# Performance work log

Measured on AMD Instinct MI355X. Metric: run time of the kernel, lower is better.

## Reference

```python
import jax, jax.numpy as jnp
import numpy as np
import itertools

RANKS_HIGH = 15
SUITS_HIGH = 5
B, M = 16, 24
# Omaha unspool: choose 2 of 4 hole cards x choose 3 of 5 board cards -> 60 five-card combos
COMBOS = np.array([h + b for h in itertools.combinations(range(4), 2)
                   for b in itertools.combinations(range(4, 9), 3)], dtype=np.int32)  # [60, 5]


def setup_inputs() -> dict:
    key = jax.random.key(0)
    ks = list(jax.random.split(key, 20))
    f = lambda i, shape: jax.random.normal(ks[i], shape, jnp.float32) * 0.05
    ranks = jax.random.randint(ks[0], (B, M, 9), 2, RANKS_HIGH)  # card ranks 2..14
    suits = jax.random.randint(ks[1], (B, M, 9), 1, SUITS_HIGH)  # suits 1..4
    x = jnp.stack([ranks, suits], axis=-1).reshape(B, M, 18)     # alternating rank/suit
    ones16 = jnp.ones((16,), jnp.float32)
    zeros16 = jnp.zeros((16,), jnp.float32)
    return {
        "x": x,
        "suit_w": f(2, (16, 5, 1)), "suit_b": f(3, (16,)),
        "rank_w": f(4, (16, 5, 5)), "rank_b": f(5, (16,)),
        "bn_s_gamma": ones16, "bn_s_beta": zeros16, "bn_s_mean": zeros16, "bn_s_var": ones16,
        "bn_r_gamma": ones16, "bn_r_beta": zeros16, "bn_r_mean": zeros16, "bn_r_var": ones16,
        "w1": f(6, (32, 16)), "b1": f(7, (32,)),
        "w2": f(8, (32, 32)), "b2": f(9, (32,)),
        "wc": f(10, (7463, 512)), "bc": f(11, (7463,)),
        "wo1": f(12, (512, 15360)), "bo1": f(13, (512,)),
        "wo2": f(14, (256, 512)), "bo2": f(15, (256,)),
        "wo3": f(16, (127, 256)), "bo3": f(17, (127,)),
    }


def _bn(t, gamma, beta, mean, var, eps=1e-5):
    # eval-mode BatchNorm1d; channel axis is -2 (shape [..., 16, L])
    inv = gamma / jnp.sqrt(var + eps)
    return t * inv[:, None] + (beta - mean * inv)[:, None]


def _forward(x, suit_w, suit_b, bn_s_gamma, bn_s_beta, bn_s_mean, bn_s_var,
             rank_w, rank_b, bn_r_gamma, bn_r_beta, bn_r_mean, bn_r_var,
             w1, b1, w2, b2, wc, bc, wo1, bo1, wo2, bo2, wo3, bo3):
    b, m, _ = x.shape
    ranks = x[..., 0::2][..., COMBOS]  # [B,M,60,5]
    suits = x[..., 1::2][..., COMBOS]  # [B,M,60,5]
    hot_r = jax.nn.one_hot(ranks, RANKS_HIGH, dtype=jnp.float32)  # [B,M,60,5,15]
    hot_s = jax.nn.one_hot(suits, SUITS_HIGH, dtype=jnp.float32)  # [B,M,60,5,5]
    # suit conv: Conv1d(5,16,k=1) over the one-hot length; channels = 5 cards
    s = jnp.einsum('bmkcl,oc->bmkol', hot_s, suit_w[:, :, 0]) + suit_b[:, None]
    s = jax.nn.relu(_bn(s, bn_s_gamma, bn_s_beta, bn_s_mean, bn_s_var))  # [B,M,60,16,5]
    # rank conv: Conv1d(5,16,k=5) valid: length 15 -> 11
    n = b * m * 60
    r = jax.lax.conv_general_dilated(hot_r.reshape(n, 5, RANKS_HIGH), rank_w,
                                     window_strides=(1,), padding='VALID',
                                     dimension_numbers=('NCH', 'OIH', 'NCH'))
    r = r.reshape(b, m, 60, 16, 11) + rank_b[:, None]
    r = jax.nn.relu(_bn(r, bn_r_gamma, bn_r_beta, bn_r_mean, bn_r_var))  # [B,M,60,16,11]
    raw = jnp.concatenate([r, s], axis=-1)  # [B,M,60,16,16]
    # hand-class head: two hidden linears on last dim, then 512 -> 7463
    h = jax.nn.relu(raw @ w1.T + b1)        # [B,M,60,16,32]
    h = jax.nn.relu(h @ w2.T + b2)          # [B,M,60,16,32]
    logits = h.reshape(b, m, 60, 512) @ wc.T + bc  # [B,M,60,7463]
    best = jnp.min(jnp.argmax(jax.lax.stop_gradient(logits), axis=-1),
                   axis=-1, keepdims=True)  # [B,M,1] (lower class index = better hand)
    # raw-feature head: [B,M,60*16*16=15360] -> 512 -> 256 -> 127
    o = raw.reshape(b, m, 60 * 16 * 16)
    o = jax.nn.relu(o @ wo1.T + bo1)
    o = jax.nn.relu(o @ wo2.T + bo2)
    o = jax.nn.relu(o @ wo3.T + bo3)
    return jnp.concatenate([o, best.astype(o.dtype)], axis=-1)  # [B,M,128]


def reference(x, suit_w, suit_b, bn_s_gamma, bn_s_beta, bn_s_mean, bn_s_var,
              rank_w, rank_b, bn_r_gamma, bn_r_beta, bn_r_mean, bn_r_var,
              w1, b1, w2, b2, wc, bc, wo1, bo1, wo2, bo2, wo3, bo3):
    return _forward(x, suit_w, suit_b, bn_s_gamma, bn_s_beta, bn_s_mean, bn_s_var,
                    rank_w, rank_b, bn_r_gamma, bn_r_beta, bn_r_mean, bn_r_var,
                    w1, b1, w2, b2, wc, bc, wo1, bo1, wo2, bo2, wo3, bo3)
```

## Files before the change

kernel.cpp:

```cpp
#include <hip/hip_runtime.h>

#define NSAMP 384
#define NCOMBO 60
#define NROW 23040
#define KDIM 512
#define NCLS 7463
#define NCLSP 7680
#define NTILE_N 60
#define NTILE_M 180
#define O1_NZ 30
#define O1_KZ 512

typedef short s16x8 __attribute__((ext_vector_type(8)));
typedef short s16x4 __attribute__((ext_vector_type(4)));
typedef float f32x4 __attribute__((ext_vector_type(4)));

__device__ unsigned short g_wc_hi[NCLSP * KDIM];
__device__ unsigned short g_wc_lo[NCLSP * KDIM];
__device__ unsigned short g_h_hi[NROW * KDIM];
__device__ unsigned short g_h_lo[NROW * KDIM];
__device__ unsigned short g_rawbf[NROW * 256];
__device__ unsigned short g_wo1bf[512 * 15360];
__device__ float          g_pmax[NTILE_N * NROW];
__device__ int            g_pidx[NTILE_N * NROW];
__device__ float          g_part[O1_NZ * NSAMP * 512];

__device__ __forceinline__ float bf2f(unsigned short u){
  union { unsigned int i; float f; } v; v.i = ((unsigned int)u) << 16; return v.f;
}
__device__ __forceinline__ unsigned short f2bf(float f){
  union { float f; unsigned int i; } v; v.f = f;
  unsigned int u = v.i;
  unsigned int r = (u + 0x7FFFu + ((u >> 16) & 1u)) >> 16;
  return (unsigned short)r;
}
__device__ __forceinline__ void gload16(const void* g, void* l){
  __builtin_amdgcn_global_load_lds((const __attribute__((address_space(1))) void*)g,
                                   (__attribute__((address_space(3))) void*)l, 16, 0, 0);
}

__global__ __launch_bounds__(256) void k_split(const float* __restrict__ wc)
{
  int idx = (blockIdx.x * 256 + threadIdx.x) * 4;
  float4 w = {0.f, 0.f, 0.f, 0.f};
  if (idx < NCLS * KDIM) w = *(const float4*)(wc + idx);
  s16x4 hi, lo;
  float wv[4] = {w.x, w.y, w.z, w.w};
  #pragma unroll
  for (int i = 0; i < 4; ++i){
    unsigned short h = f2bf(wv[i]);
    hi[i] = (short)h;
    lo[i] = (short)f2bf(wv[i] - bf2f(h));
  }
  *(s16x4*)(g_wc_hi + idx) = hi;
  *(s16x4*)(g_wc_lo + idx) = lo;
}

__global__ __launch_bounds__(256) void k_splitw(const float* __restrict__ wo1)
{
  int idx = (blockIdx.x * 256 + threadIdx.x) * 4;
  float4 w = *(const float4*)(wo1 + idx);
  s16x4 b;
  b[0] = (short)f2bf(w.x); b[1] = (short)f2bf(w.y);
  b[2] = (short)f2bf(w.z); b[3] = (short)f2bf(w.w);
  *(s16x4*)(g_wo1bf + idx) = b;
}

__global__ __launch_bounds__(256) void k_features(
    const int* __restrict__ x,
    const float* __restrict__ suit_w, const float* __restrict__ suit_b,
    const float* __restrict__ rank_w, const float* __restrict__ rank_b,
    const float* __restrict__ bns_g, const float* __restrict__ bns_b,
    const float* __restrict__ bns_m, const float* __restrict__ bns_v,
    const float* __restrict__ bnr_g, const float* __restrict__ bnr_b,
    const float* __restrict__ bnr_m, const float* __restrict__ bnr_v,
    const float* __restrict__ w1, const float* __restrict__ b1,
    const float* __restrict__ w2, const float* __restrict__ b2)
{
  __shared__ float raw_s[4][256];
  __shared__ float h1_s[4][512];
  const int tid  = threadIdx.x;
  const int lane = tid & 63;
  const int wv   = tid >> 6;
  const int combo = blockIdx.x * 4 + wv;
  const int s = combo / 60;
  const int k = combo % 60;
  const int hp = k / 10, bt = k % 10;
  const int HP0[6]  = {0,0,0,1,1,2}, HP1[6] = {1,2,3,2,3,3};
  const int BT0[10] = {4,4,4,4,4,4,5,5,5,6};
  const int BT1[10] = {5,5,5,6,6,7,6,6,7,7};
  const int BT2[10] = {6,7,8,7,8,8,7,8,8,8};
  int cards[5] = {HP0[hp], HP1[hp], BT0[bt], BT1[bt], BT2[bt]};
  const int* xp = x + s * 18;
  int rk[5], st[5];
  #pragma unroll
  for (int c = 0; c < 5; ++c){ rk[c] = xp[2*cards[c]]; st[c] = xp[2*cards[c] + 1]; }

  {
    s16x4 rv;
    #pragma unroll
    for (int i = 0; i < 4; ++i){
      int e = lane * 4 + i;
      int o = e >> 4, l = e & 15;
      float v;
      if (l < 11){
        float a = 0.f;
        #pragma unroll
        for (int c = 0; c < 5; ++c){
          int d = rk[c] - l;
          if (d >= 0 && d < 5) a += rank_w[o*25 + c*5 + d];
        }
        a += rank_b[o];
        float inv = bnr_g[o] / sqrtf(bnr_v[o] + 1e-5f);
        v = a * inv + (bnr_b[o] - bnr_m[o] * inv);
      } else {
        int j = l - 11;
        float a = suit_b[o];
        #pragma unroll
        for (int c = 0; c < 5; ++c) if (st[c] == j) a += suit_w[o*5 + c];
        float inv = bns_g[o] / sqrtf(bns_v[o] + 1e-5f);
        v = a * inv + (bns_b[o] - bns_m[o] * inv);
      }
      v = fmaxf(v, 0.f);
      raw_s[wv][e] = v;
      rv[i] = (short)f2bf(v);
    }
    *(s16x4*)(g_rawbf + (size_t)s * 15360 + k * 256 + lane * 4) = rv;
  }
  __syncthreads();
  #pragma unroll
  for (int i = 0; i < 8; ++i){
    int e = lane + 64 * i;
    int o = e >> 5, j = e & 31;
    float a = b1[j];
    #pragma unroll
    for (int l = 0; l < 16; ++l) a += raw_s[wv][o*16 + l] * w1[j*16 + l];
    h1_s[wv][e] = fmaxf(a, 0.f);
  }
  __syncthreads();
  {
    s16x8 hv, lv;
    #pragma unroll
    for (int i = 0; i < 8; ++i){
      int e = lane * 8 + i;
      int o = e >> 5, j = e & 31;
      float a = b2[j];
      #pragma unroll
      for (int l = 0; l < 32; ++l) a += h1_s[wv][o*32 + l] * w2[j*32 + l];
      a = fmaxf(a, 0.f);
      unsigned short h = f2bf(a);
      hv[i] = (short)h;
      lv[i] = (short)f2bf(a - bf2f(h));
    }
    *(s16x8*)(g_h_hi + (size_t)combo * 512 + lane * 8) = hv;
    *(s16x8*)(g_h_lo + (size_t)combo * 512 + lane * 8) = lv;
  }
}

__global__ __launch_bounds__(256, 2) void k_logits(const float* __restrict__ bc)
{
  __shared__ unsigned char lds[65536];
  const int tid  = threadIdx.x;
  const int lane = tid & 63;
  const int wv   = tid >> 6;
  const int wr   = wv >> 1, wq = wv & 1;
  const int flat  = blockIdx.x;
  const int xcd   = flat & 7;
  const int seq   = flat >> 3;
  const int group = xcd >> 1;
  const int par   = xcd & 1;
  const int mt    = (seq / 15) * 2 + par;
  const int nt    = group * 15 + (seq % 15);
  const int m0 = mt * 128;
  const int n0 = nt * 128;

  f32x4 acc[4][4];
  #pragma unroll
  for (int i = 0; i < 4; ++i)
    #pragma unroll
    for (int j = 0; j < 4; ++j)
      acc[i][j] = (f32x4){0.f, 0.f, 0.f, 0.f};

  const int rA = lane >> 2;
  const int c0 = lane & 3;

  auto stage = [&](int b, int kc){
    unsigned base = b * 32768;
    #pragma unroll
    for (int it = 0; it < 2; ++it){
      int seg = wv * 2 + it;
      int r   = seg * 16 + rA;
      int cs  = c0 ^ ((rA >> 1) & 3);
      size_t gA = (size_t)(m0 + r) * KDIM + kc + cs * 8;
      size_t gB = (size_t)(n0 + r) * KDIM + kc + cs * 8;
      unsigned lb = base + seg * 1024;
      gload16(g_h_hi  + gA, lds + lb);
      gload16(g_h_lo  + gA, lds + lb + 8192);
      gload16(g_wc_hi + gB, lds + lb + 16384);
      gload16(g_wc_lo + gB, lds + lb + 24576);
    }
  };

  int buf = 0;
  stage(0, 0);
  __syncthreads();
  for (int t = 0; t < 16; ++t){
    if (t < 15) stage(buf ^ 1, (t + 1) * 32);
    unsigned base = buf * 32768;
    const int q = lane >> 4;
    s16x8 a_h[4], a_l[4];
    #pragma unroll
    for (int i = 0; i < 4; ++i){
      int row = wr * 64 + i * 16 + (lane & 15);
      unsigned off = base + row * 64 + ((q ^ ((row >> 1) & 3)) * 16);
      a_h[i] = *(const s16x8*)(lds + off);
      a_l[i] = *(const s16x8*)(lds + off + 8192);
    }
    #pragma unroll
    for (int j = 0; j < 4; ++j){
      int col = wq * 64 + j * 16 + (lane & 15);
      unsigned off = base + col * 64 + ((q ^ ((col >> 1) & 3)) * 16);
      s16x8 b_h = *(const s16x8*)(lds + off + 16384);
      s16x8 b_l = *(const s16x8*)(lds + off + 24576);
      #pragma unroll
      for (int i = 0; i < 4; ++i){
        acc[i][j] = __builtin_amdgcn_mfma_f32_16x16x32_bf16(a_h[i], b_h, acc[i][j], 0, 0, 0);
        acc[i][j] = __builtin_amdgcn_mfma_f32_16x16x32_bf16(a_h[i], b_l, acc[i][j], 0, 0, 0);
        acc[i][j] = __builtin_amdgcn_mfma_f32_16x16x32_bf16(a_l[i], b_h, acc[i][j], 0, 0, 0);
      }
    }
    __syncthreads();
    buf ^= 1;
  }
  float* cmax = (float*)lds;
  int*   cidx = (int*)(lds + 1024);
  const int g = lane >> 4;
  #pragma unroll
  for (int i = 0; i < 4; ++i){
    #pragma unroll
    for (int r = 0; r < 4; ++r){
      float bv = -__builtin_inff(); int bi = 0x7FFFFFFF;
      #pragma unroll
      for (int j = 0; j < 4; ++j){
        int col = n0 + wq * 64 + j * 16 + (lane & 15);
        if (col < NCLS){
          float v = acc[i][j][r] + bc[col];
          if (v > bv){ bv = v; bi = col; }
        }
      }
      for (int s = 1; s < 16; s <<= 1){
        float ov = __shfl_xor(bv, s);
        int   oi = __shfl_xor(bi, s);
        if (ov > bv || (ov == bv && oi < bi)){ bv = ov; bi = oi; }
      }
      if ((lane & 15) == 0){
        int rloc = wr * 64 + i * 16 + g * 4 + r;
        cmax[rloc * 2 + wq] = bv;
        cidx[rloc * 2 + wq] = bi;
      }
    }
  }
  __syncthreads();
  if (tid < 128){
    float bv = cmax[tid * 2];     int bi = cidx[tid * 2];
    float v1 = cmax[tid * 2 + 1]; int i1 = cidx[tid * 2 + 1];
    if (v1 > bv || (v1 == bv && i1 < bi)){ bv = v1; bi = i1; }
    size_t row = (size_t)(m0 + tid);
    g_pmax[(size_t)nt * NROW + row] = bv;
    g_pidx[(size_t)nt * NROW + row] = bi;
  }
}

__global__ __launch_bounds__(64) void k_best(float* __restrict__ out)
{
  __shared__ int bis[60];
  const int s = blockIdx.x; const int t = threadIdx.x;
  if (t < 60){
    size_t row = (size_t)s * 60 + t;
    float bv = -__builtin_inff(); int bi = 0x7FFFFFFF;
    for (int q = 0; q < NTILE_N; ++q){
      float v = g_pmax[(size_t)q * NROW + row];
      int   i = g_pidx[(size_t)q * NROW + row];
      if (v > bv || (v == bv && i < bi)){ bv = v; bi = i; }
    }
    bis[t] = bi;
  }
  __syncthreads();
  if (t == 0){
    int m = bis[0];
    for (int i = 1; i < 60; ++i) m = min(m, bis[i]);
    out[s * 128 + 127] = (float)m;
  }
}

__global__ __launch_bounds__(256) void k_o1(void)
{
  __shared__ unsigned char As[16384];
  __shared__ unsigned char Bs[16384];
  const int tid  = threadIdx.x;
  const int lane = tid & 63;
  const int wv   = tid >> 6;
  const int wr   = wv >> 1, wq = wv & 1;
  const int n0  = blockIdx.x * 128;
  const int m0  = blockIdx.y * 128;
  const int kc0 = blockIdx.z * O1_KZ;

  f32x4 acc[4][4];
  #pragma unroll
  for (int i = 0; i < 4; ++i)
    #pragma unroll
    for (int j = 0; j < 4; ++j)
      acc[i][j] = (f32x4){0.f, 0.f, 0.f, 0.f};

  const int rA = lane >> 3;
  const int c0 = lane & 7;
  for (int kk = 0; kk < O1_KZ; kk += 64){
    int kc = kc0 + kk;
    __syncthreads();
    #pragma unroll
    for (int it = 0; it < 4; ++it){
      int seg = wv * 4 + it;
      int r   = seg * 8 + rA;
      int cs  = c0 ^ (r & 7);
      gload16(g_rawbf + (size_t)(m0 + r) * 15360 + kc + cs * 8, As + seg * 1024);
      gload16(g_wo1bf + (size_t)(n0 + r) * 15360 + kc + cs * 8, Bs + seg * 1024);
    }
    __syncthreads();
    #pragma unroll
    for (int ks = 0; ks < 2; ++ks){
      int q = ks * 4 + (lane >> 4);
      s16x8 a[4];
      #pragma unroll
      for (int i = 0; i < 4; ++i){
        int row = wr * 64 + i * 16 + (lane & 15);
        a[i] = *(const s16x8*)(As + row * 128 + ((q ^ (row & 7)) * 16));
      }
      #pragma unroll
      for (int j = 0; j < 4; ++j){
        int col = wq * 64 + j * 16 + (lane & 15);
        s16x8 b = *(const s16x8*)(Bs + col * 128 + ((q ^ (col & 7)) * 16));
        #pragma unroll
        for (int i = 0; i < 4; ++i)
          acc[i][j] = __builtin_amdgcn_mfma_f32_16x16x32_bf16(a[i], b, acc[i][j], 0, 0, 0);
      }
    }
  }
  const int g = lane >> 4;
  #pragma unroll
  for (int i = 0; i < 4; ++i)
    #pragma unroll
    for (int j = 0; j < 4; ++j)
      #pragma unroll
      for (int r = 0; r < 4; ++r){
        int gm = m0 + wr * 64 + i * 16 + g * 4 + r;
        int gn = n0 + wq * 64 + j * 16 + (lane & 15);
        g_part[((size_t)blockIdx.z * NSAMP + gm) * 512 + gn] = acc[i][j][r];
      }
}

__global__ __launch_bounds__(256) void k_otail(
    const float* __restrict__ bo1, const float* __restrict__ wo2,
    const float* __restrict__ bo2, const float* __restrict__ wo3,
    const float* __restrict__ bo3, float* __restrict__ out)
{
  __shared__ float o1f[512];
  __shared__ float o2f[256];
  const int s = blockIdx.x;
  const int tid = threadIdx.x;
  for (int j = tid; j < 512; j += 256){
    float a = bo1[j];
    for (int ks = 0; ks < O1_NZ; ++ks) a += g_part[((size_t)ks * NSAMP + s) * 512 + j];
    o1f[j] = fmaxf(a, 0.f);
  }
  __syncthreads();
  {
    float a = bo2[tid];
    const float* wr = wo2 + (size_t)tid * 512;
    for (int i = 0; i < 512; i += 4){
      float4 w4 = *(const float4*)(wr + i);
      a += o1f[i]*w4.x + o1f[i+1]*w4.y + o1f[i+2]*w4.z + o1f[i+3]*w4.w;
    }
    o2f[tid] = fmaxf(a, 0.f);
  }
  __syncthreads();
  if (tid < 127){
    float a = bo3[tid];
    const float* wr = wo3 + (size_t)tid * 256;
    for (int i = 0; i < 256; i += 4){
      float4 w4 = *(const float4*)(wr + i);
      a += o2f[i]*w4.x + o2f[i+1]*w4.y + o2f[i+2]*w4.z + o2f[i+3]*w4.w;
    }
    out[s * 128 + tid] = fmaxf(a, 0.f);
  }
}

extern "C" void kernel_launch(void* const* d_in, const int* in_sizes, int n_in,
                              void* d_out, int out_size, void* d_ws, size_t ws_size,
                              hipStream_t stream)
{
  (void)d_ws; (void)ws_size; (void)in_sizes; (void)n_in; (void)out_size;
  const int*   x      = (const int*)  d_in[0];
  const float* suit_w = (const float*)d_in[1];
  const float* suit_b = (const float*)d_in[2];
  const float* rank_w = (const float*)d_in[3];
  const float* rank_b = (const float*)d_in[4];
  const float* bns_g  = (const float*)d_in[5];
  const float* bns_b  = (const float*)d_in[6];
  const float* bns_m  = (const float*)d_in[7];
  const float* bns_v  = (const float*)d_in[8];
  const float* bnr_g  = (const float*)d_in[9];
  const float* bnr_b  = (const float*)d_in[10];
  const float* bnr_m  = (const float*)d_in[11];
  const float* bnr_v  = (const float*)d_in[12];
  const float* w1     = (const float*)d_in[13];
  const float* b1     = (const float*)d_in[14];
  const float* w2     = (const float*)d_in[15];
  const float* b2     = (const float*)d_in[16];
  const float* wc     = (const float*)d_in[17];
  const float* bc     = (const float*)d_in[18];
  const float* wo1    = (const float*)d_in[19];
  const float* bo1    = (const float*)d_in[20];
  const float* wo2    = (const float*)d_in[21];
  const float* bo2    = (const float*)d_in[22];
  const float* wo3    = (const float*)d_in[23];
  const float* bo3    = (const float*)d_in[24];
  float* out = (float*)d_out;

  hipLaunchKernelGGL(k_split,  dim3(3840), dim3(256), 0, stream, wc);
  hipLaunchKernelGGL(k_splitw, dim3(7680), dim3(256), 0, stream, wo1);
  hipLaunchKernelGGL(k_features, dim3(5760), dim3(256), 0, stream, x,
                     suit_w, suit_b, rank_w, rank_b,
                     bns_g, bns_b, bns_m, bns_v, bnr_g, bnr_b, bnr_m, bnr_v,
                     w1, b1, w2, b2);
  hipLaunchKernelGGL(k_logits, dim3(NTILE_N * NTILE_M), dim3(256), 0, stream, bc);
  hipLaunchKernelGGL(k_best, dim3(NSAMP), dim3(64), 0, stream, out);
  hipLaunchKernelGGL(k_o1, dim3(4, 3, O1_NZ), dim3(256), 0, stream);
  hipLaunchKernelGGL(k_otail, dim3(NSAMP), dim3(256), 0, stream,
                     bo1, wo2, bo2, wo3, bo3, out);
}
```

Baseline: 1.158 ms.

## Enlarge logits GEMM tiles to 256x256 with 8 waves and split-bf16 as K-extension

The logits GEMM moves from 128x128 tiles with 4 waves to 256x256 tiles with 8 waves. The three bf16 hi/lo partial products are recast as a K dimension three times as long (48 steps), so each step does one MFMA per fragment pair instead of staging hi and lo buffers together. Pipelining now uses explicit vmcnt waits, raw s_barrier and setprio around the MFMA block, and the argmax reduction is widened to four column waves. The goal is more operand reuse per LDS byte and less global traffic. In exchange there is higher register pressure from 32 accumulators per lane, and 2700 blocks of 512 threads may fill the CUs unevenly.

Result: no change. 1.156 ms (-0.2%).

```diff
diff --git a/kernel.cpp b/kernel.cpp
--- a/kernel.cpp
+++ b/kernel.cpp
@@ -6,8 +6,8 @@
 #define KDIM 512
 #define NCLS 7463
 #define NCLSP 7680
-#define NTILE_N 60
-#define NTILE_M 180
+#define NTILE_N 30
+#define NTILE_M 90
 #define O1_NZ 30
 #define O1_KZ 512
 
@@ -157,92 +157,102 @@
   }
 }
 
-__global__ __launch_bounds__(256, 2) void k_logits(const float* __restrict__ bc)
+__global__ __launch_bounds__(512, 2) void k_logits(const float* __restrict__ bc)
 {
   __shared__ unsigned char lds[65536];
   const int tid  = threadIdx.x;
   const int lane = tid & 63;
   const int wv   = tid >> 6;
-  const int wr   = wv >> 1, wq = wv & 1;
-  const int flat  = blockIdx.x;
-  const int xcd   = flat & 7;
-  const int seq   = flat >> 3;
-  const int group = xcd >> 1;
-  const int par   = xcd & 1;
-  const int mt    = (seq / 15) * 2 + par;
-  const int nt    = group * 15 + (seq % 15);
-  const int m0 = mt * 128;
-  const int n0 = nt * 128;
-
-  f32x4 acc[4][4];
-  #pragma unroll
-  for (int i = 0; i < 4; ++i)
+  const int wm   = wv >> 2, wn = wv & 3;
+  const int blk  = blockIdx.x;
+  const int nt   = blk / NTILE_M;
+  const int mt   = blk % NTILE_M;
+  const int m0 = mt * 256;
+  const int n0 = nt * 256;
+
+  f32x4 acc[8][4];
+  #pragma unroll
+  for (int i = 0; i < 8; ++i)
     #pragma unroll
     for (int j = 0; j < 4; ++j)
       acc[i][j] = (f32x4){0.f, 0.f, 0.f, 0.f};
 
-  const int rA = lane >> 2;
-  const int c0 = lane & 3;
-
-  auto stage = [&](int b, int kc){
-    unsigned base = b * 32768;
+  const int sR0 = tid >> 2;
+  const int sCS = (tid & 3) ^ ((tid >> 3) & 3);
+  auto stage = [&](int buf, int t){
+    const int seg = t >> 4;
+    const int kc  = (t & 15) * 32;
+    const unsigned short* As = (seg < 2) ? g_h_hi : g_h_lo;
+    const unsigned short* Bs = (seg == 1) ? g_wc_lo : g_wc_hi;
+    const unsigned base = buf * 32768;
     #pragma unroll
     for (int it = 0; it < 2; ++it){
-      int seg = wv * 2 + it;
-      int r   = seg * 16 + rA;
-      int cs  = c0 ^ ((rA >> 1) & 3);
-      size_t gA = (size_t)(m0 + r) * KDIM + kc + cs * 8;
-      size_t gB = (size_t)(n0 + r) * KDIM + kc + cs * 8;
-      unsigned lb = base + seg * 1024;
-      gload16(g_h_hi  + gA, lds + lb);
-      gload16(g_h_lo  + gA, lds + lb + 8192);
-      gload16(g_wc_hi + gB, lds + lb + 16384);
-      gload16(g_wc_lo + gB, lds + lb + 24576);
+      int R = it * 128 + sR0;
+      gload16(As + (size_t)(m0 + R) * KDIM + kc + sCS * 8,
+              lds + base + it * 8192 + wv * 1024);
+    }
+    #pragma unroll
+    for (int it = 0; it < 2; ++it){
+      int R = it * 128 + sR0;
+      gload16(Bs + (size_t)(n0 + R) * KDIM + kc + sCS * 8,
+              lds + base + 16384 + it * 8192 + wv * 1024);
     }
   };
 
-  int buf = 0;
   stage(0, 0);
-  __syncthreads();
-  for (int t = 0; t < 16; ++t){
-    if (t < 15) stage(buf ^ 1, (t + 1) * 32);
-    unsigned base = buf * 32768;
-    const int q = lane >> 4;
-    s16x8 a_h[4], a_l[4];
-    #pragma unroll
-    for (int i = 0; i < 4; ++i){
-      int row = wr * 64 + i * 16 + (lane & 15);
-      unsigned off = base + row * 64 + ((q ^ ((row >> 1) & 3)) * 16);
-      a_h[i] = *(const s16x8*)(lds + off);
-      a_l[i] = *(const s16x8*)(lds + off + 8192);
+  stage(1, 1);
+  asm volatile("s_waitcnt vmcnt(4)" ::: "memory");
+  __builtin_amdgcn_sched_barrier(0);
+  __builtin_amdgcn_s_barrier();
+  asm volatile("" ::: "memory");
+
+  const int q = lane >> 4;
+  #pragma unroll 1
+  for (int t = 0; t < 48; ++t){
+    const unsigned cb = (unsigned)(t & 1) * 32768;
+    s16x8 af[8], bf[4];
+    #pragma unroll
+    for (int i = 0; i < 8; ++i){
+      int row = wm * 128 + i * 16 + (lane & 15);
+      af[i] = *(const s16x8*)(lds + cb + row * 64 + ((q ^ ((row >> 1) & 3)) << 4));
     }
     #pragma unroll
     for (int j = 0; j < 4; ++j){
-      int col = wq * 64 + j * 16 + (lane & 15);
-      unsigned off = base + col * 64 + ((q ^ ((col >> 1) & 3)) * 16);
-      s16x8 b_h = *(const s16x8*)(lds + off + 16384);
-      s16x8 b_l = *(const s16x8*)(lds + off + 24576);
-      #pragma unroll
-      for (int i = 0; i < 4; ++i){
-        acc[i][j] = __builtin_amdgcn_mfma_f32_16x16x32_bf16(a_h[i], b_h, acc[i][j], 0, 0, 0);
-        acc[i][j] = __builtin_amdgcn_mfma_f32_16x16x32_bf16(a_h[i], b_l, acc[i][j], 0, 0, 0);
-        acc[i][j] = __builtin_amdgcn_mfma_f32_16x16x32_bf16(a_l[i], b_h, acc[i][j], 0, 0, 0);
-      }
-    }
-    __syncthreads();
-    buf ^= 1;
-  }
+      int row = wn * 64 + j * 16 + (lane & 15);
+      bf[j] = *(const s16x8*)(lds + cb + 16384 + row * 64 + ((q ^ ((row >> 1) & 3)) << 4));
+    }
+    __builtin_amdgcn_s_setprio(1);
+    #pragma unroll
+    for (int i = 0; i < 8; ++i)
+      #pragma unroll
+      for (int j = 0; j < 4; ++j)
+        acc[i][j] = __builtin_amdgcn_mfma_f32_16x16x32_bf16(af[i], bf[j], acc[i][j], 0, 0, 0);
+    __builtin_amdgcn_s_setprio(0);
+    __builtin_amdgcn_sched_barrier(0);
+    __builtin_amdgcn_s_barrier();
+    asm volatile("" ::: "memory");
+    if (t + 2 < 48){
+      stage(t & 1, t + 2);
+      asm volatile("s_waitcnt vmcnt(4)" ::: "memory");
+    } else {
+      asm volatile("s_waitcnt vmcnt(0)" ::: "memory");
+    }
+    __builtin_amdgcn_sched_barrier(0);
+    __builtin_amdgcn_s_barrier();
+    asm volatile("" ::: "memory");
+  }
+
   float* cmax = (float*)lds;
-  int*   cidx = (int*)(lds + 1024);
+  int*   cidx = (int*)(lds + 4096);
   const int g = lane >> 4;
   #pragma unroll
-  for (int i = 0; i < 4; ++i){
+  for (int i = 0; i < 8; ++i){
     #pragma unroll
     for (int r = 0; r < 4; ++r){
       float bv = -__builtin_inff(); int bi = 0x7FFFFFFF;
       #pragma unroll
       for (int j = 0; j < 4; ++j){
-        int col = n0 + wq * 64 + j * 16 + (lane & 15);
+        int col = n0 + wn * 64 + j * 16 + (lane & 15);
         if (col < NCLS){
           float v = acc[i][j][r] + bc[col];
           if (v > bv){ bv = v; bi = col; }
@@ -254,17 +264,20 @@
         if (ov > bv || (ov == bv && oi < bi)){ bv = ov; bi = oi; }
       }
       if ((lane & 15) == 0){
-        int rloc = wr * 64 + i * 16 + g * 4 + r;
-        cmax[rloc * 2 + wq] = bv;
-        cidx[rloc * 2 + wq] = bi;
-      }
-    }
-  }
-  __syncthreads();
-  if (tid < 128){
-    float bv = cmax[tid * 2];     int bi = cidx[tid * 2];
-    float v1 = cmax[tid * 2 + 1]; int i1 = cidx[tid * 2 + 1];
-    if (v1 > bv || (v1 == bv && i1 < bi)){ bv = v1; bi = i1; }
+        int rloc = wm * 128 + i * 16 + g * 4 + r;
+        cmax[rloc * 4 + wn] = bv;
+        cidx[rloc * 4 + wn] = bi;
+      }
+    }
+  }
+  __syncthreads();
+  if (tid < 256){
+    float bv = cmax[tid * 4]; int bi = cidx[tid * 4];
+    #pragma unroll
+    for (int wq = 1; wq < 4; ++wq){
+      float v = cmax[tid * 4 + wq]; int i1 = cidx[tid * 4 + wq];
+      if (v > bv || (v == bv && i1 < bi)){ bv = v; bi = i1; }
+    }
     size_t row = (size_t)(m0 + tid);
     g_pmax[(size_t)nt * NROW + row] = bv;
     g_pidx[(size_t)nt * NROW + row] = bi;
@@ -432,7 +445,7 @@
                      suit_w, suit_b, rank_w, rank_b,
                      bns_g, bns_b, bns_m, bns_v, bnr_g, bnr_b, bnr_m, bnr_v,
                      w1, b1, w2, b2);
-  hipLaunchKernelGGL(k_logits, dim3(NTILE_N * NTILE_M), dim3(256), 0, stream, bc);
+  hipLaunchKernelGGL(k_logits, dim3(NTILE_N * NTILE_M), dim3(512), 0, stream, bc);
   hipLaunchKernelGGL(k_best, dim3(NSAMP), dim3(64), 0, stream, out);
   hipLaunchKernelGGL(k_o1, dim3(4, 3, O1_NZ), dim3(256), 0, stream);
   hipLaunchKernelGGL(k_otail, dim3(NSAMP), dim3(256), 0, stream,
```
